# Kernel optimization log

Hardware: AMD Instinct MI355X
Metric: run time of the kernel (lower is better)

Reference implementation:

```python
import jax, jax.numpy as jnp
import numpy as np

BATCH, SEQ, DMODEL, NSTATE = 4, 2048, 1024, 16


def setup_inputs() -> dict:
    key = jax.random.key(0)
    ks = jax.random.split(key, 6)
    def lin_w(k, out_d, in_d):
        # torch Linear default init scale ~ 1/sqrt(in_d)
        return jax.random.uniform(k, (out_d, in_d), jnp.float32, -1.0, 1.0) / np.sqrt(in_d).astype(np.float32)
    return {
        "x": jax.random.normal(ks[0], (BATCH, SEQ, DMODEL), jnp.float32),
        "W1": lin_w(ks[1], DMODEL, DMODEL), "b1": jnp.zeros((DMODEL,), jnp.float32),
        "W2": lin_w(ks[2], NSTATE, DMODEL), "b2": jnp.zeros((NSTATE,), jnp.float32),
        "W3": lin_w(ks[3], NSTATE, DMODEL), "b3": jnp.zeros((NSTATE,), jnp.float32),
        # A: xavier_uniform over (d_model, state_size)
        "A": jax.random.uniform(ks[4], (DMODEL, NSTATE), jnp.float32, -1.0, 1.0) * np.sqrt(6.0 / (DMODEL + NSTATE)).astype(np.float32),
    }


def reference(x, W1, b1, W2, b2, W3, b3, A):
    # Projections (bld -> bln / bld)
    Bmat = x @ W2.T + b2                      # (b, l, n)
    Cmat = x @ W3.T + b3                      # (b, l, n)
    delta = jax.nn.softplus(x @ W1.T + b1)    # (b, l, d)
    # Original math (flag=0 path):
    #   dB[b,l,d,n] = delta[b,l,d] * B[b,l,n]
    #   dA = exp(einsum('bld,dn->bldn', delta, A))  -- multiplied by a zeros h, so it
    #        contributes nothing to the output (dead math; A receives zero grad).
    #   h  = dA * 0 + x[...,None] * dB
    #   y  = einsum('bln,bldn->bld', C, h)
    # This reduces exactly to: y = x * delta * sum_n(B * C)
    bc = jnp.einsum('bln,bln->bl', Bmat, Cmat)  # (b, l)
    y = x * delta * bc[..., None]               # (b, l, d)
    return y
```

## Files before the change

### kernel.cpp

```cpp
#include <hip/hip_runtime.h>
#include <hip/hip_bf16.h>
#include <cmath>

#define BATCH 4
#define SEQ 2048
#define DM 1024
#define NS 16
#define M_ROWS (BATCH * SEQ)

typedef short bf16x8 __attribute__((ext_vector_type(8)));
typedef short bf16x4 __attribute__((ext_vector_type(4)));
typedef float f32x4 __attribute__((ext_vector_type(4)));

__device__ __forceinline__ short f2bf(float f) {
    union { float f; unsigned u; } a; a.f = f;
    unsigned u = a.u;
    return (short)((u + 0x7fffu + ((u >> 16) & 1u)) >> 16);
}
__device__ __forceinline__ float bf2f(unsigned short s) {
    union { unsigned u; float f; } a; a.u = ((unsigned)s) << 16;
    return a.f;
}

#define LDS_CAST(p) ((__attribute__((address_space(3))) unsigned*)(p))
#define GLB_CAST(p) ((const __attribute__((address_space(1))) unsigned*)(p))

__global__ void __launch_bounds__(256) convert_all(
    const float* __restrict__ x,  const float* __restrict__ W1,
    const float* __restrict__ W2, const float* __restrict__ W3,
    short* __restrict__ xb, short* __restrict__ W1b, short* __restrict__ Wcb)
{
    const int b = blockIdx.x;
    const int t = threadIdx.x;
    const float4* src; bf16x4* dst; int qbase;
    if (b < 2048)      { src = (const float4*)x;  dst = (bf16x4*)xb;  qbase = b * 1024; }
    else if (b < 2304) { src = (const float4*)W1; dst = (bf16x4*)W1b; qbase = (b - 2048) * 1024; }
    else if (b < 2308) { src = (const float4*)W2; dst = (bf16x4*)Wcb; qbase = (b - 2304) * 1024; }
    else               { src = (const float4*)W3; dst = (bf16x4*)(Wcb + NS * DM); qbase = (b - 2308) * 1024; }
    #pragma unroll
    for (int i = 0; i < 4; i++) {
        int q = qbase + i * 256 + t;
        float4 v = src[q];
        bf16x4 s;
        s.x = f2bf(v.x); s.y = f2bf(v.y); s.z = f2bf(v.z); s.w = f2bf(v.w);
        dst[q] = s;
    }
}

__global__ void __launch_bounds__(256) gemm_fused(
    const short* __restrict__ xb, const short* __restrict__ W1b,
    const short* __restrict__ Wcb, const float* __restrict__ b1,
    const float* __restrict__ b2,  const float* __restrict__ b3,
    float* __restrict__ out)
{
    __shared__ short As[128][64];
    __shared__ short Bs[128][64];
    __shared__ short Wcs[32][64];
    __shared__ float bcs[128];

    const int n0 = blockIdx.x * 128;
    const int m0 = blockIdx.y * 128;
    const int t = threadIdx.x;
    const int lane = t & 63;
    const int w = t >> 6;
    const int wm = (w >> 1) * 64;
    const int wn = (w & 1) * 64;
    const int lm = lane & 15;
    const int quad = lane >> 4;

    const int sr  = t >> 3;
    const int sc  = t & 7;
    const int gch = (sc ^ (sr & 7)) * 8;

    const short* pa = xb  + (size_t)(m0 + sr) * DM + gch;
    const short* pb = W1b + (size_t)(n0 + sr) * DM + gch;
    const short* pw = Wcb + (size_t)sr        * DM + gch;

    f32x4 acc[4][4] = {};
    f32x4 abc[2][2] = {};

    #pragma unroll
    for (int kk = 0; kk < 16; kk++) {
        const int ke = kk * 64;
        #pragma unroll
        for (int u = 0; u < 4; u++) {
            __builtin_amdgcn_global_load_lds(GLB_CAST(pa + (size_t)u * 32 * DM + ke),
                LDS_CAST(&As[u * 32 + sr][sc * 8]), 16, 0, 0);
            __builtin_amdgcn_global_load_lds(GLB_CAST(pb + (size_t)u * 32 * DM + ke),
                LDS_CAST(&Bs[u * 32 + sr][sc * 8]), 16, 0, 0);
        }
        __builtin_amdgcn_global_load_lds(GLB_CAST(pw + ke),
            LDS_CAST(&Wcs[sr][sc * 8]), 16, 0, 0);
        __syncthreads();

        #pragma unroll
        for (int ks = 0; ks < 2; ks++) {
            const int cs = ((ks * 4 + quad) ^ (lm & 7)) * 8;
            bf16x8 af[4], bfv[4], wcv[2];
            #pragma unroll
            for (int i = 0; i < 4; i++)
                af[i] = *(const bf16x8*)&As[wm + i * 16 + lm][cs];
            #pragma unroll
            for (int j = 0; j < 4; j++)
                bfv[j] = *(const bf16x8*)&Bs[wn + j * 16 + lm][cs];
            #pragma unroll
            for (int h = 0; h < 2; h++)
                wcv[h] = *(const bf16x8*)&Wcs[h * 16 + lm][cs];

            #pragma unroll
            for (int i = 0; i < 4; i++)
                #pragma unroll
                for (int j = 0; j < 4; j++)
                    acc[i][j] = __builtin_amdgcn_mfma_f32_16x16x32_bf16(
                        af[i], bfv[j], acc[i][j], 0, 0, 0);

            if (w & 1) {
                #pragma unroll
                for (int h = 0; h < 2; h++) {
                    abc[0][h] = __builtin_amdgcn_mfma_f32_16x16x32_bf16(
                        af[2], wcv[h], abc[0][h], 0, 0, 0);
                    abc[1][h] = __builtin_amdgcn_mfma_f32_16x16x32_bf16(
                        af[3], wcv[h], abc[1][h], 0, 0, 0);
                }
            } else {
                #pragma unroll
                for (int h = 0; h < 2; h++) {
                    abc[0][h] = __builtin_amdgcn_mfma_f32_16x16x32_bf16(
                        af[0], wcv[h], abc[0][h], 0, 0, 0);
                    abc[1][h] = __builtin_amdgcn_mfma_f32_16x16x32_bf16(
                        af[1], wcv[h], abc[1][h], 0, 0, 0);
                }
            }
        }
        __syncthreads();
    }

    float bb2 = b2[lm], bb3 = b3[lm];
    #pragma unroll
    for (int i2 = 0; i2 < 2; i2++) {
        #pragma unroll
        for (int r = 0; r < 4; r++) {
            float p = (abc[i2][0][r] + bb2) * (abc[i2][1][r] + bb3);
            p += __shfl_xor(p, 1);
            p += __shfl_xor(p, 2);
            p += __shfl_xor(p, 4);
            p += __shfl_xor(p, 8);
            if (lm == 0) bcs[wm + (w & 1) * 32 + i2 * 16 + quad * 4 + r] = p;
        }
    }
    __syncthreads();

    const unsigned short* xbu = (const unsigned short*)xb;
    float b1v[4];
    #pragma unroll
    for (int j = 0; j < 4; j++) b1v[j] = b1[n0 + wn + j * 16 + lm];

    #pragma unroll
    for (int i = 0; i < 4; i++) {
        #pragma unroll
        for (int r = 0; r < 4; r++) {
            int lrow = wm + i * 16 + quad * 4 + r;
            int gm = m0 + lrow;
            float bcv = bcs[lrow];
            const unsigned short* xrow = xbu + (size_t)gm * DM + n0 + wn + lm;
            float* orow = out + (size_t)gm * DM + n0 + wn + lm;
            #pragma unroll
            for (int j = 0; j < 4; j++) {
                float z = acc[i][j][r] + b1v[j];
                float az = __builtin_fabsf(z);
                float sp = fmaxf(z, 0.f) + __logf(1.f + __expf(-az));
                orow[j * 16] = bf2f(xrow[j * 16]) * sp * bcv;
            }
        }
    }
}

extern "C" void kernel_launch(void* const* d_in, const int* in_sizes, int n_in,
                              void* d_out, int out_size, void* d_ws, size_t ws_size,
                              hipStream_t stream) {
    const float* x  = (const float*)d_in[0];
    const float* W1 = (const float*)d_in[1];
    const float* b1 = (const float*)d_in[2];
    const float* W2 = (const float*)d_in[3];
    const float* b2 = (const float*)d_in[4];
    const float* W3 = (const float*)d_in[5];
    const float* b3 = (const float*)d_in[6];
    float* out = (float*)d_out;

    char* ws = (char*)d_ws;
    short* xb  = (short*)(ws);
    short* W1b = (short*)(ws + (size_t)16 * 1024 * 1024);
    short* Wcb = (short*)(ws + (size_t)18 * 1024 * 1024);

    convert_all<<<2312, 256, 0, stream>>>(x, W1, W2, W3, xb, W1b, Wcb);

    dim3 grid(DM / 128, M_ROWS / 128);
    gemm_fused<<<grid, 256, 0, stream>>>(xb, W1b, Wcb, b1, b2, b3, out);
}
```

Baseline: 123.6 us.

## Double-buffer LDS tiles to overlap global-to-LDS loads with MFMA compute

Doubles the LDS buffers for the x, W1 and Wc tiles. The next K tile is issued with global_load_lds into the spare buffer while MFMAs run on the current one, and the barrier before the loads is dropped. This is meant to hide global-memory latency behind matrix compute instead of stalling on every tile. In exchange the kernel uses about twice the LDS, which may cap blocks per CU, and the wait for the prefetch still lands at the end-of-iteration barrier.

```diff
diff --git a/kernel.cpp b/kernel.cpp
--- a/kernel.cpp
+++ b/kernel.cpp
@@ -53,9 +53,9 @@
     const float* __restrict__ b2,  const float* __restrict__ b3,
     float* __restrict__ out)
 {
-    __shared__ short As[128][64];
-    __shared__ short Bs[128][64];
-    __shared__ short Wcs[32][64];
+    __shared__ short As[2][128][64];
+    __shared__ short Bs[2][128][64];
+    __shared__ short Wcs[2][32][64];
     __shared__ float bcs[128];
 
     const int n0 = blockIdx.x * 128;
@@ -79,19 +79,26 @@
     f32x4 acc[4][4] = {};
     f32x4 abc[2][2] = {};
 
+    auto stage = [&](int buf, int kt) {
+        const int ke = kt * 64;
+        #pragma unroll
+        for (int u = 0; u < 4; u++) {
+            __builtin_amdgcn_global_load_lds(GLB_CAST(pa + (size_t)(u * 32) * DM + ke),
+                LDS_CAST(&As[buf][u * 32 + sr][sc * 8]), 16, 0, 0);
+            __builtin_amdgcn_global_load_lds(GLB_CAST(pb + (size_t)(u * 32) * DM + ke),
+                LDS_CAST(&Bs[buf][u * 32 + sr][sc * 8]), 16, 0, 0);
+        }
+        __builtin_amdgcn_global_load_lds(GLB_CAST(pw + ke),
+            LDS_CAST(&Wcs[buf][sr][sc * 8]), 16, 0, 0);
+    };
+
+    stage(0, 0);
+    __syncthreads();
+
     #pragma unroll
     for (int kk = 0; kk < 16; kk++) {
-        const int ke = kk * 64;
-        #pragma unroll
-        for (int u = 0; u < 4; u++) {
-            __builtin_amdgcn_global_load_lds(GLB_CAST(pa + (size_t)u * 32 * DM + ke),
-                LDS_CAST(&As[u * 32 + sr][sc * 8]), 16, 0, 0);
-            __builtin_amdgcn_global_load_lds(GLB_CAST(pb + (size_t)u * 32 * DM + ke),
-                LDS_CAST(&Bs[u * 32 + sr][sc * 8]), 16, 0, 0);
-        }
-        __builtin_amdgcn_global_load_lds(GLB_CAST(pw + ke),
-            LDS_CAST(&Wcs[sr][sc * 8]), 16, 0, 0);
-        __syncthreads();
+        const int cur = kk & 1;
+        if (kk < 15) stage(cur ^ 1, kk + 1);
 
         #pragma unroll
         for (int ks = 0; ks < 2; ks++) {
@@ -99,13 +106,13 @@
             bf16x8 af[4], bfv[4], wcv[2];
             #pragma unroll
             for (int i = 0; i < 4; i++)
-                af[i] = *(const bf16x8*)&As[wm + i * 16 + lm][cs];
+                af[i] = *(const bf16x8*)&As[cur][wm + i * 16 + lm][cs];
             #pragma unroll
             for (int j = 0; j < 4; j++)
-                bfv[j] = *(const bf16x8*)&Bs[wn + j * 16 + lm][cs];
+                bfv[j] = *(const bf16x8*)&Bs[cur][wn + j * 16 + lm][cs];
             #pragma unroll
             for (int h = 0; h < 2; h++)
-                wcv[h] = *(const bf16x8*)&Wcs[h * 16 + lm][cs];
+                wcv[h] = *(const bf16x8*)&Wcs[cur][h * 16 + lm][cs];
 
             #pragma unroll
             for (int i = 0; i < 4; i++)
@@ -132,7 +139,7 @@
                 }
             }
         }
-        __syncthreads();
+        if (kk < 15) __syncthreads();
     }
 
     float bb2 = b2[lm], bb3 = b3[lm];
```

Result: slower. 127.7 us (+3.3%).

## Load GEMM fragments directly from global memory, dropping LDS staging and barriers

Applied to the files above, without the earlier changes.

The LDS tiles and the global_load_lds staging are removed. Each wave now reads its MFMA operand fragments straight from global memory into registers, which also removes the per-iteration __syncthreads. Launch bounds now request two blocks per SM. The aim is to cut LDS traffic and barrier stalls, but operand reuse across waves now depends on L1/L2 caches, which multiplies global load traffic.

```diff
diff --git a/kernel.cpp b/kernel.cpp
--- a/kernel.cpp
+++ b/kernel.cpp
@@ -22,9 +22,6 @@
     return a.f;
 }
 
-#define LDS_CAST(p) ((__attribute__((address_space(3))) unsigned*)(p))
-#define GLB_CAST(p) ((const __attribute__((address_space(1))) unsigned*)(p))
-
 __global__ void __launch_bounds__(256) convert_all(
     const float* __restrict__ x,  const float* __restrict__ W1,
     const float* __restrict__ W2, const float* __restrict__ W3,
@@ -47,15 +44,12 @@
     }
 }
 
-__global__ void __launch_bounds__(256) gemm_fused(
+__global__ void __launch_bounds__(256, 2) gemm_fused(
     const short* __restrict__ xb, const short* __restrict__ W1b,
     const short* __restrict__ Wcb, const float* __restrict__ b1,
     const float* __restrict__ b2,  const float* __restrict__ b3,
     float* __restrict__ out)
 {
-    __shared__ short As[128][64];
-    __shared__ short Bs[128][64];
-    __shared__ short Wcs[32][64];
     __shared__ float bcs[128];
 
     const int n0 = blockIdx.x * 128;
@@ -68,44 +62,35 @@
     const int lm = lane & 15;
     const int quad = lane >> 4;
 
-    const int sr  = t >> 3;
-    const int sc  = t & 7;
-    const int gch = (sc ^ (sr & 7)) * 8;
-
-    const short* pa = xb  + (size_t)(m0 + sr) * DM + gch;
-    const short* pb = W1b + (size_t)(n0 + sr) * DM + gch;
-    const short* pw = Wcb + (size_t)sr        * DM + gch;
+    const short* pA[4]; const short* pB[4]; const short* pW[2];
+    #pragma unroll
+    for (int i = 0; i < 4; i++)
+        pA[i] = xb + (size_t)(m0 + wm + i * 16 + lm) * DM + quad * 8;
+    #pragma unroll
+    for (int j = 0; j < 4; j++)
+        pB[j] = W1b + (size_t)(n0 + wn + j * 16 + lm) * DM + quad * 8;
+    #pragma unroll
+    for (int h = 0; h < 2; h++)
+        pW[h] = Wcb + (size_t)(h * 16 + lm) * DM + quad * 8;
 
     f32x4 acc[4][4] = {};
     f32x4 abc[2][2] = {};
 
     #pragma unroll
     for (int kk = 0; kk < 16; kk++) {
-        const int ke = kk * 64;
-        #pragma unroll
-        for (int u = 0; u < 4; u++) {
-            __builtin_amdgcn_global_load_lds(GLB_CAST(pa + (size_t)u * 32 * DM + ke),
-                LDS_CAST(&As[u * 32 + sr][sc * 8]), 16, 0, 0);
-            __builtin_amdgcn_global_load_lds(GLB_CAST(pb + (size_t)u * 32 * DM + ke),
-                LDS_CAST(&Bs[u * 32 + sr][sc * 8]), 16, 0, 0);
-        }
-        __builtin_amdgcn_global_load_lds(GLB_CAST(pw + ke),
-            LDS_CAST(&Wcs[sr][sc * 8]), 16, 0, 0);
-        __syncthreads();
-
         #pragma unroll
         for (int ks = 0; ks < 2; ks++) {
-            const int cs = ((ks * 4 + quad) ^ (lm & 7)) * 8;
+            const int eo = kk * 64 + ks * 32;
             bf16x8 af[4], bfv[4], wcv[2];
             #pragma unroll
             for (int i = 0; i < 4; i++)
-                af[i] = *(const bf16x8*)&As[wm + i * 16 + lm][cs];
+                af[i] = *(const bf16x8*)(pA[i] + eo);
             #pragma unroll
             for (int j = 0; j < 4; j++)
-                bfv[j] = *(const bf16x8*)&Bs[wn + j * 16 + lm][cs];
+                bfv[j] = *(const bf16x8*)(pB[j] + eo);
             #pragma unroll
             for (int h = 0; h < 2; h++)
-                wcv[h] = *(const bf16x8*)&Wcs[h * 16 + lm][cs];
+                wcv[h] = *(const bf16x8*)(pW[h] + eo);
 
             #pragma unroll
             for (int i = 0; i < 4; i++)
@@ -132,7 +117,6 @@
                 }
             }
         }
-        __syncthreads();
     }
 
     float bb2 = b2[lm], bb3 = b3[lm];
```

Result: slower. 175.4 us (+42.0%).
